# Performance work log

Hardware: AMD Instinct MI355X
Metric: run time of the kernel (lower is better)

## Reference

```python
import jax, jax.numpy as jnp
import numpy as np

B, T, D, H = 8, 1024, 1024, 16

def setup_inputs() -> dict:
    key = jax.random.key(0)
    k1, k2, k3, k4, k5 = jax.random.split(key, 5)
    x = jax.random.normal(k1, (B, T, D), dtype=jnp.float32)
    mask = jnp.tril(jnp.ones((T, T), dtype=bool))[None, None]  # [1,1,T,T] causal
    s = 0.02
    W_attn = jax.random.normal(k2, (D, 3 * D), dtype=jnp.float32) * s
    b_attn = jnp.zeros((3 * D,), dtype=jnp.float32)
    W_proj = jax.random.normal(k3, (D, D), dtype=jnp.float32) * s
    b_proj = jnp.zeros((D,), dtype=jnp.float32)
    return {"x": x, "mask": mask, "W_attn": W_attn, "b_attn": b_attn,
            "W_proj": W_proj, "b_proj": b_proj}

def reference(x, mask, W_attn, b_attn, W_proj, b_proj):
    num_heads = H
    b, t, d = x.shape
    hd = d // num_heads
    qkv = x @ W_attn + b_attn                      # [b,t,3d]
    q, k, v = jnp.split(qkv, 3, axis=-1)
    def to_heads(a):
        return a.reshape(b, t, num_heads, hd).transpose(0, 2, 1, 3)  # [b,h,t,hd]
    q, k, v = to_heads(q), to_heads(k), to_heads(v)
    scale = 1.0 / jnp.sqrt(jnp.float32(hd))
    attn = jnp.einsum('bhqd,bhkd->bhqk', q, k) * scale
    attn = jnp.where(mask, attn, jnp.finfo(jnp.float32).min)
    attn = jax.nn.softmax(attn, axis=-1)
    o = jnp.einsum('bhqk,bhkd->bhqd', attn, v)
    o = o.transpose(0, 2, 1, 3).reshape(b, t, d)   # [b,t,d]
    return o @ W_proj + b_proj
```

## Files before the change

kernel.cpp:

```cpp
#include <hip/hip_runtime.h>
#include <cstdint>


typedef __attribute__((ext_vector_type(8))) short bf16x8;
typedef __attribute__((ext_vector_type(4))) float f32x4;

__device__ __forceinline__ short f2b(float x) {
  unsigned u = __builtin_bit_cast(unsigned, x);
  u += 0x7fffu + ((u >> 16) & 1u);
  return (short)(u >> 16);
}

__device__ __forceinline__ void gl2lds16(short* l, const short* g) {
  __builtin_amdgcn_global_load_lds(
      (const __attribute__((address_space(1))) void*)g,
      (__attribute__((address_space(3))) void*)l, 16, 0, 0);
}


__global__ void f32_to_bf16_vec(const float* __restrict__ in,
                                short* __restrict__ outb, int n4) {
  int i = blockIdx.x * 256 + threadIdx.x;
  if (i >= n4) return;
  float4 v = ((const float4*)in)[i];
  short4 o;
  o.x = f2b(v.x); o.y = f2b(v.y); o.z = f2b(v.z); o.w = f2b(v.w);
  ((short4*)outb)[i] = o;
}

__global__ void transpose_f32_bf16(const float* __restrict__ in,
                                   short* __restrict__ out, int R, int C) {
  __shared__ float tile[32][33];
  int c0 = blockIdx.x * 32, r0 = blockIdx.y * 32;
  int tx = threadIdx.x, ty = threadIdx.y;
#pragma unroll
  for (int i = 0; i < 32; i += 8)
    tile[ty + i][tx] = in[(long)(r0 + ty + i) * C + c0 + tx];
  __syncthreads();
#pragma unroll
  for (int i = 0; i < 32; i += 8)
    out[(long)(c0 + ty + i) * R + r0 + tx] = f2b(tile[tx][ty + i]);
}


template <int EPI>
__global__ __launch_bounds__(256, 3) void gemm_bt(
    const short* __restrict__ A, const short* __restrict__ Bt,
    const float* __restrict__ bias, float* __restrict__ outF,
    short* __restrict__ qh, short* __restrict__ kh, short* __restrict__ vT,
    int M, int N, int K) {
  __shared__ short At[128 * 64];
  __shared__ short Bl[128 * 64];
  const int t = threadIdx.x;
  const int wave = t >> 6, lane = t & 63;
  const int quad = lane >> 4, l15 = lane & 15;
  const int wr = wave >> 1, wc = wave & 1;
  const int m0 = blockIdx.y * 128, n0 = blockIdx.x * 128;

  f32x4 acc[4][4] = {};

  const int srow = t >> 3;
  const int sch0 = t & 7;

  for (int k0 = 0; k0 < K; k0 += 64) {
    __syncthreads();
#pragma unroll
    for (int c = 0; c < 4; ++c) {
      int row = c * 32 + srow;
      int ch = sch0 ^ (row & 7);
      gl2lds16(At + (c * 256 + t) * 8, A + (long)(m0 + row) * K + k0 + ch * 8);
      gl2lds16(Bl + (c * 256 + t) * 8, Bt + (long)(n0 + row) * K + k0 + ch * 8);
    }
    asm volatile("s_waitcnt vmcnt(0)" ::: "memory");
    __syncthreads();

#pragma unroll
    for (int s = 0; s < 2; ++s) {
      const int cx = (s * 4 + quad) ^ (l15 & 7);
      bf16x8 af[4], bfr[4];
#pragma unroll
      for (int i = 0; i < 4; ++i)
        af[i] = *(const bf16x8*)(At + (wr * 64 + i * 16 + l15) * 64 + cx * 8);
#pragma unroll
      for (int j = 0; j < 4; ++j)
        bfr[j] = *(const bf16x8*)(Bl + (wc * 64 + j * 16 + l15) * 64 + cx * 8);
#pragma unroll
      for (int i = 0; i < 4; ++i)
#pragma unroll
        for (int j = 0; j < 4; ++j)
          acc[i][j] = __builtin_amdgcn_mfma_f32_16x16x32_bf16(af[i], bfr[j],
                                                              acc[i][j], 0, 0, 0);
    }
  }

  if (EPI == 1) {
#pragma unroll
    for (int j = 0; j < 4; ++j) {
      int col = n0 + wc * 64 + j * 16 + l15;
      float bv = bias[col];
#pragma unroll
      for (int i = 0; i < 4; ++i)
#pragma unroll
        for (int r = 0; r < 4; ++r) {
          int row = m0 + wr * 64 + i * 16 + quad * 4 + r;
          outF[(long)row * N + col] = acc[i][j][r] + bv;
        }
    }
  } else {
    const int sec = n0 >> 10;
    const int b = m0 >> 10;
#pragma unroll
    for (int j = 0; j < 4; ++j) {
      int col = n0 + wc * 64 + j * 16 + l15;
      float bv = bias[col];
      int d = col & 1023, h = d >> 6, dh = d & 63;
      if (sec == 2) {
        long base = ((long)(b * 16 + h) * 64 + dh) * 1024;
#pragma unroll
        for (int i = 0; i < 4; ++i) {
          int tt0 = (m0 & 1023) + wr * 64 + i * 16 + quad * 4;
          short4 v;
          v.x = f2b(acc[i][j][0] + bv);
          v.y = f2b(acc[i][j][1] + bv);
          v.z = f2b(acc[i][j][2] + bv);
          v.w = f2b(acc[i][j][3] + bv);
          *(short4*)(vT + base + tt0) = v;
        }
      } else {
        short* dst = (sec == 0) ? qh : kh;
        long hbase = ((long)(b * 16 + h) * 1024) * 64 + dh;
#pragma unroll
        for (int i = 0; i < 4; ++i)
#pragma unroll
          for (int r = 0; r < 4; ++r) {
            int tt = (m0 & 1023) + wr * 64 + i * 16 + quad * 4 + r;
            dst[hbase + (long)tt * 64] = f2b(acc[i][j][r] + bv);
          }
      }
    }
  }
}


__global__ __launch_bounds__(256, 3) void attn_kernel(
    const short* __restrict__ qh, const short* __restrict__ kh,
    const short* __restrict__ vT, short* __restrict__ attout) {
  __shared__ short Kb[2][64 * 64];
  __shared__ short Vb[2][64 * 64];
  __shared__ short P_lds[2][4][16][72];
  const int pairIdx = blockIdx.x;
  const int bh = blockIdx.y;
  const int t = threadIdx.x;
  const int wave = t >> 6, lane = t & 63, quad = lane >> 4, l15 = lane & 15;
  const short* q_head = qh + (long)bh * 1024 * 64;
  const short* k_head = kh + (long)bh * 1024 * 64;
  const short* v_head = vT + (long)bh * 64 * 1024;
  const int b_ = bh >> 4, h_ = bh & 15;
  const float sl = 0.125f * 1.44269504089f;

  const int qt0 = pairIdx, qt1 = 15 - pairIdx;
  const int qb0 = qt0 * 64 + wave * 16;
  const int qb1 = qt1 * 64 + wave * 16;

  auto stage = [&](int kt, int buf) {
    const int kk0 = kt * 64;
#pragma unroll
    for (int i = 0; i < 2; ++i) {
      int s = i * 256 + t;
      int row = s >> 3, cg = (s & 7) ^ (row & 7);
      gl2lds16(&Kb[buf][s * 8], k_head + (kk0 + row) * 64 + cg * 8);
    }
#pragma unroll
    for (int i = 0; i < 2; ++i) {
      int s = i * 256 + t;
      int row = s >> 3, cg = (s & 7) ^ (row & 7);
      gl2lds16(&Vb[buf][s * 8], v_head + row * 1024 + kk0 + cg * 8);
    }
  };

  bf16x8 qf0[2], qf1[2];
#pragma unroll
  for (int s = 0; s < 2; ++s) {
    qf0[s] = *(const bf16x8*)(q_head + (qb0 + l15) * 64 + s * 32 + quad * 8);
    qf1[s] = *(const bf16x8*)(q_head + (qb1 + l15) * 64 + s * 32 + quad * 8);
  }

  float l0[4] = {0.f, 0.f, 0.f, 0.f}, l1[4] = {0.f, 0.f, 0.f, 0.f};
  f32x4 o0[4] = {}, o1[4] = {};

  stage(0, 0);
  __syncthreads();

#pragma unroll 1
  for (int kt = 0; kt <= qt1; ++kt) {
    const int buf = kt & 1;
    const short* Kt = Kb[buf];
    const short* Vt = Vb[buf];
    const bool act0 = (kt <= qt0);

    if (kt < qt1) stage(kt + 1, buf ^ 1);

    f32x4 s0[4] = {}, s1[4] = {};
#pragma unroll
    for (int jj = 0; jj < 4; ++jj) {
      int row = jj * 16 + l15;
      bf16x8 ka = *(const bf16x8*)(Kt + row * 64 + ((quad ^ (row & 7)) * 8));
      bf16x8 kb =
          *(const bf16x8*)(Kt + row * 64 + (((4 + quad) ^ (row & 7)) * 8));
      s1[jj] = __builtin_amdgcn_mfma_f32_16x16x32_bf16(qf1[0], ka, s1[jj], 0, 0, 0);
      s1[jj] = __builtin_amdgcn_mfma_f32_16x16x32_bf16(qf1[1], kb, s1[jj], 0, 0, 0);
      if (act0) {
        s0[jj] = __builtin_amdgcn_mfma_f32_16x16x32_bf16(qf0[0], ka, s0[jj], 0, 0, 0);
        s0[jj] = __builtin_amdgcn_mfma_f32_16x16x32_bf16(qf0[1], kb, s0[jj], 0, 0, 0);
      }
    }

    const bool diag1 = (kt == qt1);
#pragma unroll
    for (int jj = 0; jj < 4; ++jj) {
      int key = kt * 64 + jj * 16 + l15;
#pragma unroll
      for (int r = 0; r < 4; ++r) {
        float sv = s1[jj][r] * sl;
        if (diag1 && key > qb1 + quad * 4 + r) sv = -1e30f;
        float e = __builtin_amdgcn_exp2f(sv);
        l1[r] += e;
        P_lds[1][wave][quad * 4 + r][jj * 16 + l15] = f2b(e);
      }
    }
    if (act0) {
      const bool diag0 = (kt == qt0);
#pragma unroll
      for (int jj = 0; jj < 4; ++jj) {
        int key = kt * 64 + jj * 16 + l15;
#pragma unroll
        for (int r = 0; r < 4; ++r) {
          float sv = s0[jj][r] * sl;
          if (diag0 && key > qb0 + quad * 4 + r) sv = -1e30f;
          float e = __builtin_amdgcn_exp2f(sv);
          l0[r] += e;
          P_lds[0][wave][quad * 4 + r][jj * 16 + l15] = f2b(e);
        }
      }
    }
    asm volatile("s_waitcnt lgkmcnt(0)" ::: "memory");

    bf16x8 pf1[2], pf0[2];
#pragma unroll
    for (int s = 0; s < 2; ++s)
      pf1[s] = *(const bf16x8*)(&P_lds[1][wave][l15][s * 32 + quad * 8]);
    if (act0)
#pragma unroll
      for (int s = 0; s < 2; ++s)
        pf0[s] = *(const bf16x8*)(&P_lds[0][wave][l15][s * 32 + quad * 8]);

#pragma unroll
    for (int dj = 0; dj < 4; ++dj) {
      int row = dj * 16 + l15;
#pragma unroll
      for (int s = 0; s < 2; ++s) {
        bf16x8 vf =
            *(const bf16x8*)(Vt + row * 64 + (((s * 4 + quad) ^ (row & 7)) * 8));
        o1[dj] = __builtin_amdgcn_mfma_f32_16x16x32_bf16(pf1[s], vf, o1[dj], 0, 0, 0);
        if (act0)
          o0[dj] =
              __builtin_amdgcn_mfma_f32_16x16x32_bf16(pf0[s], vf, o0[dj], 0, 0, 0);
      }
    }
    __syncthreads();
  }

#pragma unroll
  for (int off = 1; off < 16; off <<= 1)
#pragma unroll
    for (int r = 0; r < 4; ++r) {
      l0[r] += __shfl_xor(l0[r], off);
      l1[r] += __shfl_xor(l1[r], off);
    }
  float inv0[4], inv1[4];
#pragma unroll
  for (int r = 0; r < 4; ++r) {
    inv0[r] = __builtin_amdgcn_rcpf(l0[r]);
    inv1[r] = __builtin_amdgcn_rcpf(l1[r]);
  }
#pragma unroll
  for (int dj = 0; dj < 4; ++dj)
#pragma unroll
    for (int r = 0; r < 4; ++r) {
      int col = h_ * 64 + dj * 16 + l15;
      long g0 = (long)b_ * 1024 + qb0 + quad * 4 + r;
      long g1 = (long)b_ * 1024 + qb1 + quad * 4 + r;
      attout[g0 * 1024 + col] = f2b(o0[dj][r] * inv0[r]);
      attout[g1 * 1024 + col] = f2b(o1[dj][r] * inv1[r]);
    }
}


extern "C" void kernel_launch(void* const* d_in, const int* in_sizes, int n_in,
                              void* d_out, int out_size, void* d_ws,
                              size_t ws_size, hipStream_t stream) {
  const float* x = (const float*)d_in[0];
  const float* W_attn = (const float*)d_in[2];
  const float* b_attn = (const float*)d_in[3];
  const float* W_proj = (const float*)d_in[4];
  const float* b_proj = (const float*)d_in[5];
  float* out = (float*)d_out;

  char* ws = (char*)d_ws;
  const size_t MB = 1u << 20;
  short* xb = (short*)(ws);
  short* WaT = (short*)(ws + 16 * MB);
  short* WpT = (short*)(ws + 22 * MB);
  short* qh = (short*)(ws + 24 * MB);
  short* kh = (short*)(ws + 40 * MB);
  short* vT = (short*)(ws + 56 * MB);
  short* attout = xb;

  f32_to_bf16_vec<<<8192, 256, 0, stream>>>(x, xb, 2097152);
  transpose_f32_bf16<<<dim3(3072 / 32, 1024 / 32), dim3(32, 8), 0, stream>>>(
      W_attn, WaT, 1024, 3072);
  transpose_f32_bf16<<<dim3(1024 / 32, 1024 / 32), dim3(32, 8), 0, stream>>>(
      W_proj, WpT, 1024, 1024);
  gemm_bt<0><<<dim3(3072 / 128, 8192 / 128), 256, 0, stream>>>(
      xb, WaT, b_attn, nullptr, qh, kh, vT, 8192, 3072, 1024);
  attn_kernel<<<dim3(8, 128), 256, 0, stream>>>(qh, kh, vT, attout);
  gemm_bt<1><<<dim3(1024 / 128, 8192 / 128), 256, 0, stream>>>(
      attout, WpT, b_proj, out, nullptr, nullptr, nullptr, 8192, 1024, 1024);
}
```

Baseline: 241.9 us.

## Serialize the two attention query tiles and shrink P buffer to raise occupancy

Restructures the attention inner loop so the two paired query tiles are processed one after another, reusing K fragments that are preloaded into registers. This lets a single XOR-swizzled P buffer replace the double one. Occupancy is raised from 3 to 4 blocks per SM, K reads move ahead of the next-tile prefetch, and the grid is reordered so blocks of the same head-pair index launch together. The goals are lower LDS and register pressure and more latency hiding, at the cost of less MFMA interleaving between the two tiles and possible register spills under the tighter launch bound.

```diff
diff --git a/kernel.cpp b/kernel.cpp
--- a/kernel.cpp
+++ b/kernel.cpp
@@ -142,14 +142,14 @@
 }
 
 
-__global__ __launch_bounds__(256, 3) void attn_kernel(
+__global__ __launch_bounds__(256, 4) void attn_kernel(
     const short* __restrict__ qh, const short* __restrict__ kh,
     const short* __restrict__ vT, short* __restrict__ attout) {
   __shared__ short Kb[2][64 * 64];
   __shared__ short Vb[2][64 * 64];
-  __shared__ short P_lds[2][4][16][72];
-  const int pairIdx = blockIdx.x;
-  const int bh = blockIdx.y;
+  __shared__ short P_lds[4][16][64];
+  const int bh = blockIdx.x;
+  const int pairIdx = blockIdx.y;
   const int t = threadIdx.x;
   const int wave = t >> 6, lane = t & 63, quad = lane >> 4, l15 = lane & 15;
   const short* q_head = qh + (long)bh * 1024 * 64;
@@ -198,73 +198,97 @@
     const short* Vt = Vb[buf];
     const bool act0 = (kt <= qt0);
 
-    if (kt < qt1) stage(kt + 1, buf ^ 1);
-
-    f32x4 s0[4] = {}, s1[4] = {};
+    bf16x8 kfr[4][2];
 #pragma unroll
     for (int jj = 0; jj < 4; ++jj) {
       int row = jj * 16 + l15;
-      bf16x8 ka = *(const bf16x8*)(Kt + row * 64 + ((quad ^ (row & 7)) * 8));
-      bf16x8 kb =
-          *(const bf16x8*)(Kt + row * 64 + (((4 + quad) ^ (row & 7)) * 8));
-      s1[jj] = __builtin_amdgcn_mfma_f32_16x16x32_bf16(qf1[0], ka, s1[jj], 0, 0, 0);
-      s1[jj] = __builtin_amdgcn_mfma_f32_16x16x32_bf16(qf1[1], kb, s1[jj], 0, 0, 0);
-      if (act0) {
-        s0[jj] = __builtin_amdgcn_mfma_f32_16x16x32_bf16(qf0[0], ka, s0[jj], 0, 0, 0);
-        s0[jj] = __builtin_amdgcn_mfma_f32_16x16x32_bf16(qf0[1], kb, s0[jj], 0, 0, 0);
-      }
-    }
-
-    const bool diag1 = (kt == qt1);
-#pragma unroll
-    for (int jj = 0; jj < 4; ++jj) {
-      int key = kt * 64 + jj * 16 + l15;
-#pragma unroll
-      for (int r = 0; r < 4; ++r) {
-        float sv = s1[jj][r] * sl;
-        if (diag1 && key > qb1 + quad * 4 + r) sv = -1e30f;
-        float e = __builtin_amdgcn_exp2f(sv);
-        l1[r] += e;
-        P_lds[1][wave][quad * 4 + r][jj * 16 + l15] = f2b(e);
-      }
-    }
-    if (act0) {
-      const bool diag0 = (kt == qt0);
+#pragma unroll
+      for (int s = 0; s < 2; ++s)
+        kfr[jj][s] =
+            *(const bf16x8*)(Kt + row * 64 + (((s * 4 + quad) ^ (row & 7)) * 8));
+    }
+
+    if (kt < qt1) stage(kt + 1, buf ^ 1);
+
+    {
+      f32x4 s1[4] = {};
+#pragma unroll
+      for (int jj = 0; jj < 4; ++jj) {
+        s1[jj] =
+            __builtin_amdgcn_mfma_f32_16x16x32_bf16(qf1[0], kfr[jj][0], s1[jj], 0, 0, 0);
+        s1[jj] =
+            __builtin_amdgcn_mfma_f32_16x16x32_bf16(qf1[1], kfr[jj][1], s1[jj], 0, 0, 0);
+      }
+      const bool diag1 = (kt == qt1);
 #pragma unroll
       for (int jj = 0; jj < 4; ++jj) {
         int key = kt * 64 + jj * 16 + l15;
+        int ch = jj * 2 + (l15 >> 3), co = l15 & 7;
 #pragma unroll
         for (int r = 0; r < 4; ++r) {
+          int row = quad * 4 + r;
+          float sv = s1[jj][r] * sl;
+          if (diag1 && key > qb1 + row) sv = -1e30f;
+          float e = __builtin_amdgcn_exp2f(sv);
+          l1[r] += e;
+          P_lds[wave][row][(ch ^ (row & 7)) * 8 + co] = f2b(e);
+        }
+      }
+      asm volatile("s_waitcnt lgkmcnt(0)" ::: "memory");
+      bf16x8 pf[2];
+#pragma unroll
+      for (int s = 0; s < 2; ++s)
+        pf[s] = *(const bf16x8*)(&P_lds[wave][l15][((s * 4 + quad) ^ (l15 & 7)) * 8]);
+#pragma unroll
+      for (int dj = 0; dj < 4; ++dj) {
+        int row = dj * 16 + l15;
+#pragma unroll
+        for (int s = 0; s < 2; ++s) {
+          bf16x8 vf =
+              *(const bf16x8*)(Vt + row * 64 + (((s * 4 + quad) ^ (row & 7)) * 8));
+          o1[dj] = __builtin_amdgcn_mfma_f32_16x16x32_bf16(pf[s], vf, o1[dj], 0, 0, 0);
+        }
+      }
+    }
+
+    if (act0) {
+      f32x4 s0[4] = {};
+#pragma unroll
+      for (int jj = 0; jj < 4; ++jj) {
+        s0[jj] =
+            __builtin_amdgcn_mfma_f32_16x16x32_bf16(qf0[0], kfr[jj][0], s0[jj], 0, 0, 0);
+        s0[jj] =
+            __builtin_amdgcn_mfma_f32_16x16x32_bf16(qf0[1], kfr[jj][1], s0[jj], 0, 0, 0);
+      }
+      const bool diag0 = (kt == qt0);
+#pragma unroll
+      for (int jj = 0; jj < 4; ++jj) {
+        int key = kt * 64 + jj * 16 + l15;
+        int ch = jj * 2 + (l15 >> 3), co = l15 & 7;
+#pragma unroll
+        for (int r = 0; r < 4; ++r) {
+          int row = quad * 4 + r;
           float sv = s0[jj][r] * sl;
-          if (diag0 && key > qb0 + quad * 4 + r) sv = -1e30f;
+          if (diag0 && key > qb0 + row) sv = -1e30f;
           float e = __builtin_amdgcn_exp2f(sv);
           l0[r] += e;
-          P_lds[0][wave][quad * 4 + r][jj * 16 + l15] = f2b(e);
-        }
-      }
-    }
-    asm volatile("s_waitcnt lgkmcnt(0)" ::: "memory");
-
-    bf16x8 pf1[2], pf0[2];
-#pragma unroll
-    for (int s = 0; s < 2; ++s)
-      pf1[s] = *(const bf16x8*)(&P_lds[1][wave][l15][s * 32 + quad * 8]);
-    if (act0)
+          P_lds[wave][row][(ch ^ (row & 7)) * 8 + co] = f2b(e);
+        }
+      }
+      asm volatile("s_waitcnt lgkmcnt(0)" ::: "memory");
+      bf16x8 pf[2];
 #pragma unroll
       for (int s = 0; s < 2; ++s)
-        pf0[s] = *(const bf16x8*)(&P_lds[0][wave][l15][s * 32 + quad * 8]);
-
-#pragma unroll
-    for (int dj = 0; dj < 4; ++dj) {
-      int row = dj * 16 + l15;
-#pragma unroll
-      for (int s = 0; s < 2; ++s) {
-        bf16x8 vf =
-            *(const bf16x8*)(Vt + row * 64 + (((s * 4 + quad) ^ (row & 7)) * 8));
-        o1[dj] = __builtin_amdgcn_mfma_f32_16x16x32_bf16(pf1[s], vf, o1[dj], 0, 0, 0);
-        if (act0)
-          o0[dj] =
-              __builtin_amdgcn_mfma_f32_16x16x32_bf16(pf0[s], vf, o0[dj], 0, 0, 0);
+        pf[s] = *(const bf16x8*)(&P_lds[wave][l15][((s * 4 + quad) ^ (l15 & 7)) * 8]);
+#pragma unroll
+      for (int dj = 0; dj < 4; ++dj) {
+        int row = dj * 16 + l15;
+#pragma unroll
+        for (int s = 0; s < 2; ++s) {
+          bf16x8 vf =
+              *(const bf16x8*)(Vt + row * 64 + (((s * 4 + quad) ^ (row & 7)) * 8));
+          o0[dj] = __builtin_amdgcn_mfma_f32_16x16x32_bf16(pf[s], vf, o0[dj], 0, 0, 0);
+        }
       }
     }
     __syncthreads();
@@ -323,7 +347,7 @@
       W_proj, WpT, 1024, 1024);
   gemm_bt<0><<<dim3(3072 / 128, 8192 / 128), 256, 0, stream>>>(
       xb, WaT, b_attn, nullptr, qh, kh, vT, 8192, 3072, 1024);
-  attn_kernel<<<dim3(8, 128), 256, 0, stream>>>(qh, kh, vT, attout);
+  attn_kernel<<<dim3(128, 8), 256, 0, stream>>>(qh, kh, vT, attout);
   gemm_bt<1><<<dim3(1024 / 128, 8192 / 128), 256, 0, stream>>>(
       attout, WpT, b_proj, out, nullptr, nullptr, nullptr, 8192, 1024, 1024);
 }
```

New measurement: 276.4 us. 1.14x slower.

## Process four query tiles per attention block and hoist K/V fragments to registers

Applied to the files above, without the earlier changes.

Each attention block now handles four causal query tiles (p, 7-p, 8+p, 15-p) instead of two. This halves the grid and reuses each staged K/V tile across more queries. K and V fragments are loaded into registers once per key tile, before issuing the next async stage, and the P scratch buffer gets an XOR swizzle. Output is staged through LDS for vectorized 16-byte global stores, and occupancy is relaxed to 2 blocks to fit the larger register footprint.

```diff
diff --git a/kernel.cpp b/kernel.cpp
--- a/kernel.cpp
+++ b/kernel.cpp
@@ -142,13 +142,13 @@
 }
 
 
-__global__ __launch_bounds__(256, 3) void attn_kernel(
+__global__ __launch_bounds__(256, 2) void attn_kernel(
     const short* __restrict__ qh, const short* __restrict__ kh,
     const short* __restrict__ vT, short* __restrict__ attout) {
   __shared__ short Kb[2][64 * 64];
   __shared__ short Vb[2][64 * 64];
-  __shared__ short P_lds[2][4][16][72];
-  const int pairIdx = blockIdx.x;
+  __shared__ short P_lds[4][16][64];
+  const int p = blockIdx.x;
   const int bh = blockIdx.y;
   const int t = threadIdx.x;
   const int wave = t >> 6, lane = t & 63, quad = lane >> 4, l15 = lane & 15;
@@ -158,9 +158,7 @@
   const int b_ = bh >> 4, h_ = bh & 15;
   const float sl = 0.125f * 1.44269504089f;
 
-  const int qt0 = pairIdx, qt1 = 15 - pairIdx;
-  const int qb0 = qt0 * 64 + wave * 16;
-  const int qb1 = qt1 * 64 + wave * 16;
+  const int qt[4] = {p, 7 - p, 8 + p, 15 - p};
 
   auto stage = [&](int kt, int buf) {
     const int kk0 = kt * 64;
@@ -178,121 +176,121 @@
     }
   };
 
-  bf16x8 qf0[2], qf1[2];
-#pragma unroll
-  for (int s = 0; s < 2; ++s) {
-    qf0[s] = *(const bf16x8*)(q_head + (qb0 + l15) * 64 + s * 32 + quad * 8);
-    qf1[s] = *(const bf16x8*)(q_head + (qb1 + l15) * 64 + s * 32 + quad * 8);
-  }
-
-  float l0[4] = {0.f, 0.f, 0.f, 0.f}, l1[4] = {0.f, 0.f, 0.f, 0.f};
-  f32x4 o0[4] = {}, o1[4] = {};
+  bf16x8 qf[4][2];
+#pragma unroll
+  for (int i = 0; i < 4; ++i) {
+    int qb = qt[i] * 64 + wave * 16;
+#pragma unroll
+    for (int s = 0; s < 2; ++s)
+      qf[i][s] = *(const bf16x8*)(q_head + (qb + l15) * 64 + s * 32 + quad * 8);
+  }
+
+  float l[4][4] = {};
+  f32x4 o[4][4] = {};
 
   stage(0, 0);
   __syncthreads();
 
+  const int nkt = qt[3] + 1;
+
 #pragma unroll 1
-  for (int kt = 0; kt <= qt1; ++kt) {
+  for (int kt = 0; kt < nkt; ++kt) {
     const int buf = kt & 1;
     const short* Kt = Kb[buf];
     const short* Vt = Vb[buf];
-    const bool act0 = (kt <= qt0);
-
-    if (kt < qt1) stage(kt + 1, buf ^ 1);
-
-    f32x4 s0[4] = {}, s1[4] = {};
+
+    bf16x8 kfr[4][2], vfr[4][2];
 #pragma unroll
     for (int jj = 0; jj < 4; ++jj) {
       int row = jj * 16 + l15;
-      bf16x8 ka = *(const bf16x8*)(Kt + row * 64 + ((quad ^ (row & 7)) * 8));
-      bf16x8 kb =
-          *(const bf16x8*)(Kt + row * 64 + (((4 + quad) ^ (row & 7)) * 8));
-      s1[jj] = __builtin_amdgcn_mfma_f32_16x16x32_bf16(qf1[0], ka, s1[jj], 0, 0, 0);
-      s1[jj] = __builtin_amdgcn_mfma_f32_16x16x32_bf16(qf1[1], kb, s1[jj], 0, 0, 0);
-      if (act0) {
-        s0[jj] = __builtin_amdgcn_mfma_f32_16x16x32_bf16(qf0[0], ka, s0[jj], 0, 0, 0);
-        s0[jj] = __builtin_amdgcn_mfma_f32_16x16x32_bf16(qf0[1], kb, s0[jj], 0, 0, 0);
+#pragma unroll
+      for (int s = 0; s < 2; ++s) {
+        int off = ((s * 4 + quad) ^ (row & 7)) * 8;
+        kfr[jj][s] = *(const bf16x8*)(Kt + row * 64 + off);
+        vfr[jj][s] = *(const bf16x8*)(Vt + row * 64 + off);
       }
     }
 
-    const bool diag1 = (kt == qt1);
-#pragma unroll
-    for (int jj = 0; jj < 4; ++jj) {
-      int key = kt * 64 + jj * 16 + l15;
+    if (kt + 1 < nkt) stage(kt + 1, buf ^ 1);
+
+#pragma unroll
+    for (int i = 0; i < 4; ++i) {
+      if (kt <= qt[i]) {
+        f32x4 s4[4] = {};
+#pragma unroll
+        for (int jj = 0; jj < 4; ++jj) {
+          s4[jj] = __builtin_amdgcn_mfma_f32_16x16x32_bf16(qf[i][0], kfr[jj][0],
+                                                           s4[jj], 0, 0, 0);
+          s4[jj] = __builtin_amdgcn_mfma_f32_16x16x32_bf16(qf[i][1], kfr[jj][1],
+                                                           s4[jj], 0, 0, 0);
+        }
+        const bool diag = (kt == qt[i]);
+        const int qb = qt[i] * 64 + wave * 16;
+#pragma unroll
+        for (int jj = 0; jj < 4; ++jj) {
+          int key = kt * 64 + jj * 16 + l15;
+          int ch = jj * 2 + (l15 >> 3), co = l15 & 7;
+#pragma unroll
+          for (int r = 0; r < 4; ++r) {
+            int row = quad * 4 + r;
+            float sv = s4[jj][r] * sl;
+            if (diag && key > qb + row) sv = -1e30f;
+            float e = __builtin_amdgcn_exp2f(sv);
+            l[i][r] += e;
+            P_lds[wave][row][(ch ^ (row & 7)) * 8 + co] = f2b(e);
+          }
+        }
+        asm volatile("s_waitcnt lgkmcnt(0)" ::: "memory");
+        bf16x8 pf[2];
+#pragma unroll
+        for (int s = 0; s < 2; ++s)
+          pf[s] =
+              *(const bf16x8*)(&P_lds[wave][l15][((s * 4 + quad) ^ (l15 & 7)) * 8]);
+#pragma unroll
+        for (int dj = 0; dj < 4; ++dj) {
+          o[i][dj] = __builtin_amdgcn_mfma_f32_16x16x32_bf16(pf[0], vfr[dj][0],
+                                                             o[i][dj], 0, 0, 0);
+          o[i][dj] = __builtin_amdgcn_mfma_f32_16x16x32_bf16(pf[1], vfr[dj][1],
+                                                             o[i][dj], 0, 0, 0);
+        }
+      }
+    }
+    __syncthreads();
+  }
+
+#pragma unroll
+  for (int off = 1; off < 16; off <<= 1)
+#pragma unroll
+    for (int i = 0; i < 4; ++i)
+#pragma unroll
+      for (int r = 0; r < 4; ++r) l[i][r] += __shfl_xor(l[i][r], off);
+
+  const int erow = lane >> 3, ech = lane & 7;
+#pragma unroll
+  for (int i = 0; i < 4; ++i) {
+    float inv[4];
+#pragma unroll
+    for (int r = 0; r < 4; ++r) inv[r] = __builtin_amdgcn_rcpf(l[i][r]);
+    const int qb = qt[i] * 64 + wave * 16;
+#pragma unroll
+    for (int dj = 0; dj < 4; ++dj) {
+      int ch = dj * 2 + (l15 >> 3), co = l15 & 7;
 #pragma unroll
       for (int r = 0; r < 4; ++r) {
-        float sv = s1[jj][r] * sl;
-        if (diag1 && key > qb1 + quad * 4 + r) sv = -1e30f;
-        float e = __builtin_amdgcn_exp2f(sv);
-        l1[r] += e;
-        P_lds[1][wave][quad * 4 + r][jj * 16 + l15] = f2b(e);
+        int row = quad * 4 + r;
+        P_lds[wave][row][(ch ^ (row & 7)) * 8 + co] = f2b(o[i][dj][r] * inv[r]);
       }
     }
-    if (act0) {
-      const bool diag0 = (kt == qt0);
-#pragma unroll
-      for (int jj = 0; jj < 4; ++jj) {
-        int key = kt * 64 + jj * 16 + l15;
-#pragma unroll
-        for (int r = 0; r < 4; ++r) {
-          float sv = s0[jj][r] * sl;
-          if (diag0 && key > qb0 + quad * 4 + r) sv = -1e30f;
-          float e = __builtin_amdgcn_exp2f(sv);
-          l0[r] += e;
-          P_lds[0][wave][quad * 4 + r][jj * 16 + l15] = f2b(e);
-        }
-      }
-    }
     asm volatile("s_waitcnt lgkmcnt(0)" ::: "memory");
-
-    bf16x8 pf1[2], pf0[2];
-#pragma unroll
-    for (int s = 0; s < 2; ++s)
-      pf1[s] = *(const bf16x8*)(&P_lds[1][wave][l15][s * 32 + quad * 8]);
-    if (act0)
-#pragma unroll
-      for (int s = 0; s < 2; ++s)
-        pf0[s] = *(const bf16x8*)(&P_lds[0][wave][l15][s * 32 + quad * 8]);
-
-#pragma unroll
-    for (int dj = 0; dj < 4; ++dj) {
-      int row = dj * 16 + l15;
-#pragma unroll
-      for (int s = 0; s < 2; ++s) {
-        bf16x8 vf =
-            *(const bf16x8*)(Vt + row * 64 + (((s * 4 + quad) ^ (row & 7)) * 8));
-        o1[dj] = __builtin_amdgcn_mfma_f32_16x16x32_bf16(pf1[s], vf, o1[dj], 0, 0, 0);
-        if (act0)
-          o0[dj] =
-              __builtin_amdgcn_mfma_f32_16x16x32_bf16(pf0[s], vf, o0[dj], 0, 0, 0);
-      }
-    }
-    __syncthreads();
-  }
-
-#pragma unroll
-  for (int off = 1; off < 16; off <<= 1)
-#pragma unroll
-    for (int r = 0; r < 4; ++r) {
-      l0[r] += __shfl_xor(l0[r], off);
-      l1[r] += __shfl_xor(l1[r], off);
-    }
-  float inv0[4], inv1[4];
-#pragma unroll
-  for (int r = 0; r < 4; ++r) {
-    inv0[r] = __builtin_amdgcn_rcpf(l0[r]);
-    inv1[r] = __builtin_amdgcn_rcpf(l1[r]);
-  }
-#pragma unroll
-  for (int dj = 0; dj < 4; ++dj)
-#pragma unroll
-    for (int r = 0; r < 4; ++r) {
-      int col = h_ * 64 + dj * 16 + l15;
-      long g0 = (long)b_ * 1024 + qb0 + quad * 4 + r;
-      long g1 = (long)b_ * 1024 + qb1 + quad * 4 + r;
-      attout[g0 * 1024 + col] = f2b(o0[dj][r] * inv0[r]);
-      attout[g1 * 1024 + col] = f2b(o1[dj][r] * inv1[r]);
-    }
+#pragma unroll
+    for (int pass = 0; pass < 2; ++pass) {
+      int row = pass * 8 + erow;
+      bf16x8 v = *(const bf16x8*)(&P_lds[wave][row][(ech ^ (row & 7)) * 8]);
+      long g = (long)b_ * 1024 + qb + row;
+      *(bf16x8*)(attout + g * 1024 + h_ * 64 + ech * 8) = v;
+    }
+    asm volatile("s_waitcnt lgkmcnt(0)" ::: "memory");
+  }
 }
 
 
@@ -323,7 +321,7 @@
       W_proj, WpT, 1024, 1024);
   gemm_bt<0><<<dim3(3072 / 128, 8192 / 128), 256, 0, stream>>>(
       xb, WaT, b_attn, nullptr, qh, kh, vT, 8192, 3072, 1024);
-  attn_kernel<<<dim3(8, 128), 256, 0, stream>>>(qh, kh, vT, attout);
+  attn_kernel<<<dim3(4, 128), 256, 0, stream>>>(qh, kh, vT, attout);
   gemm_bt<1><<<dim3(1024 / 128, 8192 / 128), 256, 0, stream>>>(
       attout, WpT, b_proj, out, nullptr, nullptr, nullptr, 8192, 1024, 1024);
 }
```

Result: faster. 230.5 us (-4.7%).
